# Optimization experiments

Hardware: AMD Instinct MI355X
Metric: run time of the kernel (lower is better)

## Reference

```python
import jax, jax.numpy as jnp
import numpy as np

B, L, D, F, T = 32, 768, 256, 256, 3072
_EPS = 1e-5


def _layernorm(h, g, b):
    mu = jnp.mean(h, axis=-1, keepdims=True)
    var = jnp.var(h, axis=-1, keepdims=True)
    return (h - mu) * jax.lax.rsqrt(var + _EPS) * g + b


def _conv1d(h, w, b):
    # h: [B, L, Cin], w: [K, Cin, Cout] (HIO), padding=1 matches torch Conv1d(padding=1)
    return jax.lax.conv_general_dilated(h, w, (1,), [(1, 1)], dimension_numbers=('NHC', 'HIO', 'NHC')) + b


def setup_inputs() -> dict:
    key = jax.random.key(0)
    ks = jax.random.split(key, 6)
    return {
        'x': jax.random.normal(ks[0], (B, L, D), jnp.float32),
        'target': jax.random.randint(ks[1], (B, L), 0, 4, jnp.int32),
        'mel_max_length': T,
        'conv1_w': jax.random.normal(ks[2], (3, D, F), jnp.float32) * 0.05,
        'conv1_b': jnp.zeros((F,), jnp.float32),
        'ln1_g': jnp.ones((F,), jnp.float32),
        'ln1_b': jnp.zeros((F,), jnp.float32),
        'conv2_w': jax.random.normal(ks[3], (3, F, F), jnp.float32) * 0.05,
        'conv2_b': jnp.zeros((F,), jnp.float32),
        'ln2_g': jnp.ones((F,), jnp.float32),
        'ln2_b': jnp.zeros((F,), jnp.float32),
        'lin_w': jax.random.normal(ks[4], (F, 1), jnp.float32) * 0.05,
        'lin_b': jnp.zeros((1,), jnp.float32),
    }


def reference(x, target, mel_max_length, conv1_w, conv1_b, ln1_g, ln1_b,
              conv2_w, conv2_b, ln2_g, ln2_b, lin_w, lin_b):
    alpha = 1.0
    # DurationPredictor: conv -> relu -> LN -> conv -> relu -> LN -> linear (dropout=0)
    h = _layernorm(jax.nn.relu(_conv1d(x, conv1_w, conv1_b)), ln1_g, ln1_b)
    h = _layernorm(jax.nn.relu(_conv1d(h, conv2_w, conv2_b)), ln2_g, ln2_b)
    dp_out = (h @ lin_w + lin_b)[..., 0]                       # [B, L]
    durations = jnp.exp(dp_out) * alpha                        # [B, L] float
    # Training branch: durations come from target
    dpo = jnp.round(target.astype(jnp.float32) * alpha).astype(jnp.int32)  # [B, L]
    # LR: alignment @ x realized as cumulative-duration searchsorted + gather
    cum = jnp.cumsum(dpo, axis=1)                              # [B, L]
    t = jnp.arange(mel_max_length, dtype=jnp.int32)            # [T]
    idx = jax.vmap(lambda c: jnp.searchsorted(c, t, side='right'))(cum)  # [B, T]
    mask = (t[None, :] < cum[:, -1:]).astype(x.dtype)          # [B, T] zero past total frames
    out = jnp.take_along_axis(x, jnp.clip(idx, 0, x.shape[1] - 1)[:, :, None], axis=1)
    out = out * mask[:, :, None]                               # [B, T, D]
    return (out, dpo, durations)
```

## Files before the change

### kernel.cpp

```cpp
#include <hip/hip_runtime.h>
#include <hip/hip_bf16.h>
#include <math.h>

#define BB 32
#define LL 768
#define DD 256
#define FF 256
#define TT 3072
#define MT 32
#define PAD 264
#define A1R 50

typedef __attribute__((ext_vector_type(8))) short bf16x8;
typedef __attribute__((ext_vector_type(4))) float f32x4;

__device__ inline unsigned short f2b(float f) {
    union { float f; unsigned u; } v; v.f = f;
    unsigned r = (v.u + 0x7FFF + ((v.u >> 16) & 1)) >> 16;
    return (unsigned short)r;
}

__global__ __launch_bounds__(256) void prep_w_kernel(
    const float* __restrict__ w1, const float* __restrict__ w2,
    unsigned short* __restrict__ wQ1, unsigned short* __restrict__ wQ2)
{
    const int layer = blockIdx.x / 24;
    const int s  = blockIdx.x % 24;
    const int kc = s >> 3, c8 = s & 7;
    const float* __restrict__ w = layer ? w2 : w1;
    unsigned short* __restrict__ o = (layer ? wQ2 : wQ1) + s * 8192 + threadIdx.x * 32;
    const int n = threadIdx.x;

    alignas(16) unsigned short tmp[32];
#pragma unroll
    for (int q = 0; q < 4; ++q)
#pragma unroll
        for (int j = 0; j < 8; ++j) {
            const int cin = c8 * 32 + q * 8 + j;
            tmp[q * 8 + j] = f2b(w[((size_t)(kc * 256 + cin)) * 256 + n]);
        }
#pragma unroll
    for (int i = 0; i < 4; ++i)
        *reinterpret_cast<uint4*>(o + i * 8) = *reinterpret_cast<const uint4*>(tmp + i * 8);
}

__global__ __launch_bounds__(256) void fused_dp_kernel(
    const float* __restrict__ x,
    const unsigned short* __restrict__ wQ1,
    const unsigned short* __restrict__ wQ2,
    const float* __restrict__ c1b, const float* __restrict__ g1, const float* __restrict__ b1,
    const float* __restrict__ c2b, const float* __restrict__ g2, const float* __restrict__ b2,
    const float* __restrict__ lw,  const float* __restrict__ lb,
    float* __restrict__ out_dur)
{
    __shared__ union {
        unsigned short A1[A1R * PAD];
        unsigned short h2[34 * PAD];
    } sm;
    __shared__ float red[4][3][4][4][2];
    __shared__ float redp[4][2][4][4];
    __shared__ float fin[48][2];

    const int tid  = threadIdx.x;
    const int b    = blockIdx.x / (LL / MT);
    const int l0   = (blockIdx.x % (LL / MT)) * MT;
    const int wave = tid >> 6, lane = tid & 63;
    const int quad = lane >> 4, l16 = lane & 15;

    int   cols[4];
    float c1bv[4], g1v[4], b1v[4], c2bv[4], g2v[4], b2v[4], lwv[4];
#pragma unroll
    for (int nt = 0; nt < 4; ++nt) {
        const int c = wave * 64 + nt * 16 + l16;
        cols[nt] = c;
        c1bv[nt] = c1b[c]; g1v[nt] = g1[c]; b1v[nt] = b1[c];
        c2bv[nt] = c2b[c]; g2v[nt] = g2[c]; b2v[nt] = b2[c];
        lwv[nt]  = lw[c];
    }
    const float lbv = lb[0];

    {
        const int ch = (tid & 31) * 8;
        const int rr = tid >> 5;
        for (int p = 0; p < 7; ++p) {
            const int ar = p * 8 + rr;
            if (ar >= A1R) break;
            const int l = l0 - 2 + ar;
            bf16x8 val;
#pragma unroll
            for (int j = 0; j < 8; ++j) val[j] = 0;
            if (l >= 0 && l < LL) {
                const float* pp = x + ((size_t)b * LL + l) * DD + ch;
                const float4 v0 = *reinterpret_cast<const float4*>(pp);
                const float4 v1 = *reinterpret_cast<const float4*>(pp + 4);
                val[0] = (short)f2b(v0.x); val[1] = (short)f2b(v0.y);
                val[2] = (short)f2b(v0.z); val[3] = (short)f2b(v0.w);
                val[4] = (short)f2b(v1.x); val[5] = (short)f2b(v1.y);
                val[6] = (short)f2b(v1.z); val[7] = (short)f2b(v1.w);
            }
            *reinterpret_cast<bf16x8*>(&sm.A1[ar * PAD + ch]) = val;
        }
    }
    __syncthreads();

    f32x4 acc1[3][4] = {};
    for (int s = 0; s < 24; ++s) {
        const int kc = s >> 3, c8 = s & 7;
        bf16x8 a[3], bf[4];
#pragma unroll
        for (int mt = 0; mt < 3; ++mt)
            a[mt] = *reinterpret_cast<const bf16x8*>(
                &sm.A1[(16 * mt + l16 + kc) * PAD + c8 * 32 + quad * 8]);
#pragma unroll
        for (int nt = 0; nt < 4; ++nt)
            bf[nt] = *reinterpret_cast<const bf16x8*>(
                wQ1 + (size_t)s * 8192 + cols[nt] * 32 + quad * 8);
#pragma unroll
        for (int mt = 0; mt < 3; ++mt)
#pragma unroll
            for (int nt = 0; nt < 4; ++nt)
                acc1[mt][nt] = __builtin_amdgcn_mfma_f32_16x16x32_bf16(
                    a[mt], bf[nt], acc1[mt][nt], 0, 0, 0);
    }
    __syncthreads();

#pragma unroll
    for (int mt = 0; mt < 3; ++mt)
#pragma unroll
        for (int r = 0; r < 4; ++r) {
            float s1 = 0.f, s2 = 0.f;
#pragma unroll
            for (int nt = 0; nt < 4; ++nt) {
                const float v = fmaxf(acc1[mt][nt][r] + c1bv[nt], 0.f);
                s1 += v; s2 += v * v;
            }
            for (int m = 1; m < 16; m <<= 1) {
                s1 += __shfl_xor(s1, m, 64);
                s2 += __shfl_xor(s2, m, 64);
            }
            if (l16 == 0) { red[wave][mt][quad][r][0] = s1; red[wave][mt][quad][r][1] = s2; }
        }
    __syncthreads();
    if (tid < 48) {
        const int mt = tid >> 4, q = (tid >> 2) & 3, r = tid & 3;
        const float s1 = red[0][mt][q][r][0] + red[1][mt][q][r][0]
                       + red[2][mt][q][r][0] + red[3][mt][q][r][0];
        const float s2 = red[0][mt][q][r][1] + red[1][mt][q][r][1]
                       + red[2][mt][q][r][1] + red[3][mt][q][r][1];
        const float mu  = s1 * (1.f / 256.f);
        const float var = s2 * (1.f / 256.f) - mu * mu;
        fin[tid][0] = mu;
        fin[tid][1] = rsqrtf(var + 1e-5f);
    }
    __syncthreads();

#pragma unroll
    for (int mt = 0; mt < 3; ++mt)
#pragma unroll
        for (int r = 0; r < 4; ++r) {
            const int rho = 16 * mt + quad * 4 + r;
            if (rho < 34) {
                const int gr = l0 - 1 + rho;
                const float mu = fin[rho][0], rstd = fin[rho][1];
#pragma unroll
                for (int nt = 0; nt < 4; ++nt) {
                    unsigned short hv = 0;
                    if (gr >= 0 && gr < LL) {
                        const float v = fmaxf(acc1[mt][nt][r] + c1bv[nt], 0.f);
                        hv = f2b((v - mu) * rstd * g1v[nt] + b1v[nt]);
                    }
                    sm.h2[rho * PAD + cols[nt]] = hv;
                }
            }
        }
    __syncthreads();

    f32x4 acc2[2][4] = {};
    for (int s = 0; s < 24; ++s) {
        const int kc = s >> 3, c8 = s & 7;
        bf16x8 a[2], bf[4];
#pragma unroll
        for (int mt = 0; mt < 2; ++mt)
            a[mt] = *reinterpret_cast<const bf16x8*>(
                &sm.h2[(16 * mt + l16 + kc) * PAD + c8 * 32 + quad * 8]);
#pragma unroll
        for (int nt = 0; nt < 4; ++nt)
            bf[nt] = *reinterpret_cast<const bf16x8*>(
                wQ2 + (size_t)s * 8192 + cols[nt] * 32 + quad * 8);
#pragma unroll
        for (int mt = 0; mt < 2; ++mt)
#pragma unroll
            for (int nt = 0; nt < 4; ++nt)
                acc2[mt][nt] = __builtin_amdgcn_mfma_f32_16x16x32_bf16(
                    a[mt], bf[nt], acc2[mt][nt], 0, 0, 0);
    }

#pragma unroll
    for (int mt = 0; mt < 2; ++mt)
#pragma unroll
        for (int r = 0; r < 4; ++r) {
            float s1 = 0.f, s2 = 0.f;
#pragma unroll
            for (int nt = 0; nt < 4; ++nt) {
                const float v = fmaxf(acc2[mt][nt][r] + c2bv[nt], 0.f);
                s1 += v; s2 += v * v;
            }
            for (int m = 1; m < 16; m <<= 1) {
                s1 += __shfl_xor(s1, m, 64);
                s2 += __shfl_xor(s2, m, 64);
            }
            if (l16 == 0) { red[wave][mt][quad][r][0] = s1; red[wave][mt][quad][r][1] = s2; }
        }
    __syncthreads();
    if (tid < 32) {
        const int mt = tid >> 4, q = (tid >> 2) & 3, r = tid & 3;
        const float s1 = red[0][mt][q][r][0] + red[1][mt][q][r][0]
                       + red[2][mt][q][r][0] + red[3][mt][q][r][0];
        const float s2 = red[0][mt][q][r][1] + red[1][mt][q][r][1]
                       + red[2][mt][q][r][1] + red[3][mt][q][r][1];
        const float mu  = s1 * (1.f / 256.f);
        const float var = s2 * (1.f / 256.f) - mu * mu;
        fin[tid][0] = mu;
        fin[tid][1] = rsqrtf(var + 1e-5f);
    }
    __syncthreads();

#pragma unroll
    for (int mt = 0; mt < 2; ++mt)
#pragma unroll
        for (int r = 0; r < 4; ++r) {
            const int rho = 16 * mt + quad * 4 + r;
            const float mu = fin[rho][0], rstd = fin[rho][1];
            float p = 0.f;
#pragma unroll
            for (int nt = 0; nt < 4; ++nt) {
                const float v = fmaxf(acc2[mt][nt][r] + c2bv[nt], 0.f);
                p += ((v - mu) * rstd * g2v[nt] + b2v[nt]) * lwv[nt];
            }
            for (int m = 1; m < 16; m <<= 1) p += __shfl_xor(p, m, 64);
            if (l16 == 0) redp[wave][mt][quad][r] = p;
        }
    __syncthreads();
    if (tid < 32) {
        const int mt = tid >> 4, q = (tid >> 2) & 3, r = tid & 3;
        const float dp = redp[0][mt][q][r] + redp[1][mt][q][r]
                       + redp[2][mt][q][r] + redp[3][mt][q][r] + lbv;
        out_dur[(size_t)b * LL + l0 + tid] = expf(dp);
    }
}

__global__ __launch_bounds__(256) void scan_kernel(
    const int* __restrict__ target,
    float* __restrict__ out_dpo,
    int* __restrict__ idx_map)
{
    __shared__ int tsum[256];
    const int b = blockIdx.x, tid = threadIdx.x;

    const int l = 3 * tid;
    const int v0 = target[b * LL + l];
    const int v1 = target[b * LL + l + 1];
    const int v2 = target[b * LL + l + 2];
    out_dpo[b * LL + l]     = (float)v0;
    out_dpo[b * LL + l + 1] = (float)v1;
    out_dpo[b * LL + l + 2] = (float)v2;

    const int s0 = v0, s1 = v0 + v1, s2 = v0 + v1 + v2;
    tsum[tid] = s2;
    __syncthreads();
    for (int off = 1; off < 256; off <<= 1) {
        int xq = (tid >= off) ? tsum[tid - off] : 0;
        __syncthreads();
        tsum[tid] += xq;
        __syncthreads();
    }
    const int excl = tsum[tid] - s2;

    for (int t = tid; t < TT; t += 256) idx_map[b * TT + t] = -1;
    __syncthreads();

    const int c0 = excl + s0, c1 = excl + s1, c2 = excl + s2;
    for (int t = excl; t < c0 && t < TT; ++t) idx_map[b * TT + t] = l;
    for (int t = c0;   t < c1 && t < TT; ++t) idx_map[b * TT + t] = l + 1;
    for (int t = c1;   t < c2 && t < TT; ++t) idx_map[b * TT + t] = l + 2;
}

__global__ __launch_bounds__(256) void gather_kernel(
    const float* __restrict__ x,
    const int* __restrict__ idx_map,
    float* __restrict__ out)
{
    const int wv = threadIdx.x >> 6, lane = threadIdx.x & 63;
    const int row = blockIdx.x * 4 + wv;
    const int b = row / TT, t = row - b * TT;
    const int idx = idx_map[b * TT + t];
    float4 val = make_float4(0.f, 0.f, 0.f, 0.f);
    if (idx >= 0)
        val = reinterpret_cast<const float4*>(x)[(size_t)(b * LL + idx) * (DD / 4) + lane];
    reinterpret_cast<float4*>(out)[(size_t)row * (DD / 4) + lane] = val;
}

extern "C" void kernel_launch(void* const* d_in, const int* in_sizes, int n_in,
                              void* d_out, int out_size, void* d_ws, size_t ws_size,
                              hipStream_t stream)
{
    const float* x      = (const float*)d_in[0];
    const int*   target = (const int*)  d_in[1];
    const float* c1w = (const float*)d_in[3];
    const float* c1b = (const float*)d_in[4];
    const float* g1  = (const float*)d_in[5];
    const float* b1  = (const float*)d_in[6];
    const float* c2w = (const float*)d_in[7];
    const float* c2b = (const float*)d_in[8];
    const float* g2  = (const float*)d_in[9];
    const float* b2  = (const float*)d_in[10];
    const float* lw  = (const float*)d_in[11];
    const float* lb  = (const float*)d_in[12];

    float* out0    = (float*)d_out;
    float* out_dpo = out0 + (size_t)BB * TT * DD;
    float* out_dur = out_dpo + (size_t)BB * LL;

    char* ws = (char*)d_ws;
    unsigned short* wQ1 = (unsigned short*)ws;                 ws += (size_t)24 * 8192 * 2;
    unsigned short* wQ2 = (unsigned short*)ws;                 ws += (size_t)24 * 8192 * 2;
    int* idx_map        = (int*)ws;

    prep_w_kernel<<<48, 256, 0, stream>>>(c1w, c2w, wQ1, wQ2);

    fused_dp_kernel<<<BB * (LL / MT), 256, 0, stream>>>(
        x, wQ1, wQ2, c1b, g1, b1, c2b, g2, b2, lw, lb, out_dur);

    scan_kernel<<<BB, 256, 0, stream>>>(target, out_dpo, idx_map);
    gather_kernel<<<BB * TT / 4, 256, 0, stream>>>(x, idx_map, out0);
}
```

Measured before the change: 209.0 us.

## Merge gather into duration-predictor kernel so memory-bound copy overlaps compute

```diff
diff --git a/kernel.cpp b/kernel.cpp
--- a/kernel.cpp
+++ b/kernel.cpp
@@ -10,6 +10,8 @@
 #define MT 32
 #define PAD 264
 #define A1R 50
+#define FGRID (BB * (LL / MT))
+#define GGRID 1536
 
 typedef __attribute__((ext_vector_type(8))) short bf16x8;
 typedef __attribute__((ext_vector_type(4))) float f32x4;
@@ -44,14 +46,52 @@
         *reinterpret_cast<uint4*>(o + i * 8) = *reinterpret_cast<const uint4*>(tmp + i * 8);
 }
 
-__global__ __launch_bounds__(256) void fused_dp_kernel(
+__global__ __launch_bounds__(256) void scan_kernel(
+    const int* __restrict__ target,
+    float* __restrict__ out_dpo,
+    int* __restrict__ idx_map)
+{
+    __shared__ int tsum[256];
+    const int b = blockIdx.x, tid = threadIdx.x;
+
+    const int l = 3 * tid;
+    const int v0 = target[b * LL + l];
+    const int v1 = target[b * LL + l + 1];
+    const int v2 = target[b * LL + l + 2];
+    out_dpo[b * LL + l]     = (float)v0;
+    out_dpo[b * LL + l + 1] = (float)v1;
+    out_dpo[b * LL + l + 2] = (float)v2;
+
+    const int s0 = v0, s1 = v0 + v1, s2 = v0 + v1 + v2;
+    tsum[tid] = s2;
+    __syncthreads();
+    for (int off = 1; off < 256; off <<= 1) {
+        int xq = (tid >= off) ? tsum[tid - off] : 0;
+        __syncthreads();
+        tsum[tid] += xq;
+        __syncthreads();
+    }
+    const int excl = tsum[tid] - s2;
+
+    for (int t = tid; t < TT; t += 256) idx_map[b * TT + t] = -1;
+    __syncthreads();
+
+    const int c0 = excl + s0, c1 = excl + s1, c2 = excl + s2;
+    for (int t = excl; t < c0 && t < TT; ++t) idx_map[b * TT + t] = l;
+    for (int t = c0;   t < c1 && t < TT; ++t) idx_map[b * TT + t] = l + 1;
+    for (int t = c1;   t < c2 && t < TT; ++t) idx_map[b * TT + t] = l + 2;
+}
+
+__global__ __launch_bounds__(256) void mega_kernel(
     const float* __restrict__ x,
     const unsigned short* __restrict__ wQ1,
     const unsigned short* __restrict__ wQ2,
     const float* __restrict__ c1b, const float* __restrict__ g1, const float* __restrict__ b1,
     const float* __restrict__ c2b, const float* __restrict__ g2, const float* __restrict__ b2,
     const float* __restrict__ lw,  const float* __restrict__ lb,
-    float* __restrict__ out_dur)
+    const int* __restrict__ idx_map,
+    float* __restrict__ out_dur,
+    float* __restrict__ out0)
 {
     __shared__ union {
         unsigned short A1[A1R * PAD];
@@ -62,9 +102,25 @@
     __shared__ float fin[48][2];
 
     const int tid  = threadIdx.x;
+    const int wave = tid >> 6, lane = tid & 63;
+
+    if (blockIdx.x >= FGRID) {
+        const int gb = blockIdx.x - FGRID;
+        const float4* __restrict__ x4 = reinterpret_cast<const float4*>(x);
+        float4* __restrict__ o4 = reinterpret_cast<float4*>(out0);
+        for (int row = gb * 4 + wave; row < BB * TT; row += GGRID * 4) {
+            const int b = row / TT, t = row - b * TT;
+            const int idx = idx_map[b * TT + t];
+            float4 val = make_float4(0.f, 0.f, 0.f, 0.f);
+            if (idx >= 0)
+                val = x4[(size_t)(b * LL + idx) * (DD / 4) + lane];
+            o4[(size_t)row * (DD / 4) + lane] = val;
+        }
+        return;
+    }
+
     const int b    = blockIdx.x / (LL / MT);
     const int l0   = (blockIdx.x % (LL / MT)) * MT;
-    const int wave = tid >> 6, lane = tid & 63;
     const int quad = lane >> 4, l16 = lane & 15;
 
     int   cols[4];
@@ -247,57 +303,6 @@
                        + redp[2][mt][q][r] + redp[3][mt][q][r] + lbv;
         out_dur[(size_t)b * LL + l0 + tid] = expf(dp);
     }
-}
-
-__global__ __launch_bounds__(256) void scan_kernel(
-    const int* __restrict__ target,
-    float* __restrict__ out_dpo,
-    int* __restrict__ idx_map)
-{
-    __shared__ int tsum[256];
-    const int b = blockIdx.x, tid = threadIdx.x;
-
-    const int l = 3 * tid;
-    const int v0 = target[b * LL + l];
-    const int v1 = target[b * LL + l + 1];
-    const int v2 = target[b * LL + l + 2];
-    out_dpo[b * LL + l]     = (float)v0;
-    out_dpo[b * LL + l + 1] = (float)v1;
-    out_dpo[b * LL + l + 2] = (float)v2;
-
-    const int s0 = v0, s1 = v0 + v1, s2 = v0 + v1 + v2;
-    tsum[tid] = s2;
-    __syncthreads();
-    for (int off = 1; off < 256; off <<= 1) {
-        int xq = (tid >= off) ? tsum[tid - off] : 0;
-        __syncthreads();
-        tsum[tid] += xq;
-        __syncthreads();
-    }
-    const int excl = tsum[tid] - s2;
-
-    for (int t = tid; t < TT; t += 256) idx_map[b * TT + t] = -1;
-    __syncthreads();
-
-    const int c0 = excl + s0, c1 = excl + s1, c2 = excl + s2;
-    for (int t = excl; t < c0 && t < TT; ++t) idx_map[b * TT + t] = l;
-    for (int t = c0;   t < c1 && t < TT; ++t) idx_map[b * TT + t] = l + 1;
-    for (int t = c1;   t < c2 && t < TT; ++t) idx_map[b * TT + t] = l + 2;
-}
-
-__global__ __launch_bounds__(256) void gather_kernel(
-    const float* __restrict__ x,
-    const int* __restrict__ idx_map,
-    float* __restrict__ out)
-{
-    const int wv = threadIdx.x >> 6, lane = threadIdx.x & 63;
-    const int row = blockIdx.x * 4 + wv;
-    const int b = row / TT, t = row - b * TT;
-    const int idx = idx_map[b * TT + t];
-    float4 val = make_float4(0.f, 0.f, 0.f, 0.f);
-    if (idx >= 0)
-        val = reinterpret_cast<const float4*>(x)[(size_t)(b * LL + idx) * (DD / 4) + lane];
-    reinterpret_cast<float4*>(out)[(size_t)row * (DD / 4) + lane] = val;
 }
 
 extern "C" void kernel_launch(void* const* d_in, const int* in_sizes, int n_in,
@@ -327,10 +332,9 @@
     int* idx_map        = (int*)ws;
 
     prep_w_kernel<<<48, 256, 0, stream>>>(c1w, c2w, wQ1, wQ2);
-
-    fused_dp_kernel<<<BB * (LL / MT), 256, 0, stream>>>(
-        x, wQ1, wQ2, c1b, g1, b1, c2b, g2, b2, lw, lb, out_dur);
-
     scan_kernel<<<BB, 256, 0, stream>>>(target, out_dpo, idx_map);
-    gather_kernel<<<BB * TT / 4, 256, 0, stream>>>(x, idx_map, out0);
-}
+
+    mega_kernel<<<FGRID + GGRID, 256, 0, stream>>>(
+        x, wQ1, wQ2, c1b, g1, b1, c2b, g2, b2, lw, lb,
+        idx_map, out_dur, out0);
+}
```

New measurement: 203.3 us. 2.7% less time.
